# Kernel optimization log

Hardware: AMD Instinct MI355X
Metric: run time of the kernel (lower is better)

Reference implementation:

```python
import jax, jax.numpy as jnp
import numpy as np

EMBED_DIM = 256
NUM_HEADS = 8
MLP_HIDDEN = 1024
EPS = 1e-5
ROPE_BASE = 10000.0
NEG_INF = -1e9


def _ln(x, g, b):
    m = jnp.mean(x, axis=-1, keepdims=True)
    v = jnp.mean((x - m) ** 2, axis=-1, keepdims=True)
    return (x - m) / jnp.sqrt(v + EPS) * g + b


def _proj_qkv(x, W, b):
    # x: (B, L, E); W: (3E, E)
    qkv = x @ W.T + b
    q, k, v = jnp.split(qkv, 3, axis=-1)
    B, L, E = x.shape
    def h(t):
        return t.reshape(B, L, NUM_HEADS, E // NUM_HEADS).transpose(0, 2, 1, 3)
    return h(q), h(k), h(v)


def _rope(x, offset):
    # x: (B, H, L, hd), interleaved even/odd rotation
    hd = x.shape[-1]
    L = x.shape[-2]
    inv_freq = 1.0 / (ROPE_BASE ** (jnp.arange(0, hd, 2, dtype=jnp.float32) / hd))
    t = jnp.arange(L, dtype=jnp.float32) + offset
    freqs = t[:, None] * inv_freq[None, :]  # (L, hd/2)
    cos = jnp.cos(freqs)[None, None].astype(x.dtype)
    sin = jnp.sin(freqs)[None, None].astype(x.dtype)
    xe = x[..., 0::2]
    xo = x[..., 1::2]
    xr = jnp.stack((xe * cos - xo * sin, xe * sin + xo * cos), axis=-1)
    return xr.reshape(x.shape)


def _sdpa(q, k, v, bias):
    scale = 1.0 / jnp.sqrt(jnp.asarray(q.shape[-1], q.dtype))
    s = jnp.einsum('bhqd,bhkd->bhqk', q, k) * scale + bias
    p = jax.nn.softmax(s, axis=-1)
    return jnp.einsum('bhqk,bhkd->bhqd', p, v)


def _mha_self(x, in_w, in_b, out_w, out_b):
    q, k, v = _proj_qkv(x, in_w, in_b)
    o = _sdpa(q, k, v, jnp.zeros((), x.dtype))
    B, H, L, hd = o.shape
    o = o.transpose(0, 2, 1, 3).reshape(B, L, H * hd)
    return o @ out_w.T + out_b


def setup_inputs() -> dict:
    key = jax.random.key(0)
    ks = jax.random.split(key, 20)
    E, Hm = EMBED_DIM, MLP_HIDDEN
    sc = 0.02
    inp = {
        'src': jax.random.normal(ks[0], (8, 128, 64, E), dtype=jnp.float32),
        'src_mask': jax.random.randint(ks[1], (8, 128), 0, 2, dtype=jnp.int32),
        'ctx_qry_split_index': 96,
        'y_in_w': jax.random.normal(ks[2], (3 * E, E)) * sc,
        'y_in_b': jnp.zeros((3 * E,)),
        'y_out_w': jax.random.normal(ks[3], (E, E)) * sc,
        'y_out_b': jnp.zeros((E,)),
        'x_in_w': jax.random.normal(ks[4], (3 * E, E)) * sc,
        'x_in_b': jnp.zeros((3 * E,)),
        'x_out_w': jax.random.normal(ks[5], (E, E)) * sc,
        'x_out_b': jnp.zeros((E,)),
        'w1': jax.random.normal(ks[6], (Hm, E)) * sc,
        'b1': jnp.zeros((Hm,)),
        'w2': jax.random.normal(ks[7], (E, Hm)) * sc,
        'b2': jnp.zeros((E,)),
        'n1_g': jnp.ones((E,)), 'n1_b': jnp.zeros((E,)),
        'n2_g': jnp.ones((E,)), 'n2_b': jnp.zeros((E,)),
        'n3_g': jnp.ones((E,)), 'n3_b': jnp.zeros((E,)),
    }
    return inp


def reference(src, src_mask, ctx_qry_split_index,
              y_in_w, y_in_b, y_out_w, y_out_b,
              x_in_w, x_in_b, x_out_w, x_out_b,
              w1, b1, w2, b2,
              n1_g, n1_b, n2_g, n2_b, n3_g, n3_b):
    bs, R, C, E = src.shape
    S = int(ctx_qry_split_index)
    # ---- y (column-axis) self-attention ----
    x = src.reshape(bs * R, C, E)
    x = jnp.nan_to_num(x, nan=0.0, posinf=0.0, neginf=0.0)
    x = _mha_self(x, y_in_w, y_in_b, y_out_w, y_out_b) + x
    x = x.reshape(bs, R, C, E)
    x = _ln(x, n1_g, n1_b)
    # ---- x (row-axis) attention with ctx/qry split ----
    x = x.transpose(0, 2, 1, 3).reshape(bs * C, R, E)
    x = jnp.nan_to_num(x, nan=0.0, posinf=0.0, neginf=0.0)
    mask_x = jnp.broadcast_to((src_mask > 0)[:, None, :], (bs, C, R)).reshape(bs * C, R)
    kpm_ctx = ~mask_x[:, :S]  # (B, S) True = padded
    bias = jnp.where(kpm_ctx[:, None, None, :], jnp.asarray(NEG_INF, x.dtype), 0.0)
    src_ctx = x[:, :S, :]
    src_qry = x[:, S:, :]
    # ctx self-attention
    q_c, k_c, v_c = _proj_qkv(src_ctx, x_in_w, x_in_b)
    q_c = _rope(q_c, 0)
    k_c = _rope(k_c, 0)
    out_ctx = _sdpa(q_c, k_c, v_c, bias)
    B = bs * C
    out_ctx = out_ctx.transpose(0, 2, 1, 3).reshape(B, S, E)
    out_ctx = out_ctx @ x_out_w.T + x_out_b
    src_ctx = out_ctx + src_ctx
    # qry cross-attention into (updated) ctx
    q_q, _, _ = _proj_qkv(src_qry, x_in_w, x_in_b)
    _, k_c2, v_c2 = _proj_qkv(src_ctx, x_in_w, x_in_b)
    q_q = _rope(q_q, S)
    k_c2 = _rope(k_c2, 0)
    out_qry = _sdpa(q_q, k_c2, v_c2, bias)
    L_qry = R - S
    out_qry = out_qry.transpose(0, 2, 1, 3).reshape(B, L_qry, E)
    out_qry = out_qry @ x_out_w.T + x_out_b
    src_qry = out_qry + src_qry
    x = jnp.concatenate([src_ctx, src_qry], axis=1)
    x = x.reshape(bs, C, R, E).transpose(0, 2, 1, 3)
    x = _ln(x, n2_g, n2_b)
    # ---- FFN ----
    mlp = (jax.nn.gelu(x @ w1.T + b1, approximate=False)) @ w2.T + b2
    x = x + mlp
    return _ln(x, n3_g, n3_b)
```

## Files before the change

### kernel.cpp

```cpp
#include <hip/hip_runtime.h>
#include <hip/hip_bf16.h>
#include <math.h>


#define EDIM 256
#define HD   32
#define SCTX 96

typedef __bf16 bf16x8 __attribute__((ext_vector_type(8)));
typedef float  f32x4  __attribute__((ext_vector_type(4)));
union Frag { bf16x8 v; unsigned short u[8]; };

static __device__ __forceinline__ float b2f(unsigned short u) {
    return __uint_as_float(((unsigned int)u) << 16);
}
static __device__ __forceinline__ unsigned short f2b(float f) {
    unsigned int u = __float_as_uint(f);
    u += 0x7fffu + ((u >> 16) & 1u);
    return (unsigned short)(u >> 16);
}

static __device__ __forceinline__ void gload16(const unsigned short* g, unsigned short* l) {
    __builtin_amdgcn_global_load_lds(
        (const __attribute__((address_space(1))) unsigned int*)g,
        (__attribute__((address_space(3))) unsigned int*)l,
        16, 0, 0);
}

__global__ void detect_kernel(const unsigned int* __restrict__ n1g_raw,
                              int* __restrict__ flag) {
    *flag = (*n1g_raw == 0x3F800000u) ? 1 : 0;
}

struct PtrTable { const void* p[18]; };

__global__ void cvt_kernel(PtrTable t, const int* __restrict__ flag,
                           unsigned short* __restrict__ wp) {
    const int seg_off[19] = {0, 196608, 197376, 262912, 263168, 459776, 460544,
                             526080, 526336, 788480, 789504, 1051648, 1051904,
                             1052160, 1052416, 1052672, 1052928, 1053184, 1053440};
    const int f = *flag;
    int idx = blockIdx.x * blockDim.x + threadIdx.x;
    int stride = gridDim.x * blockDim.x;
    for (int i = idx; i < 1053440; i += stride) {
        int s = 0;
        while (i >= seg_off[s + 1]) ++s;
        int j = i - seg_off[s];
        unsigned short o;
        if (f) o = f2b(((const float*)t.p[s])[j]);
        else   o = ((const unsigned short*)t.p[s])[j];
        wp[i] = o;
    }
}

__global__ void rope_tab_kernel(float2* __restrict__ tab) {
    int i = blockIdx.x * blockDim.x + threadIdx.x;
    int pos = i >> 4, f = i & 15;
    float invf = exp2f((float)f * -0.8304820237193385f);
    float ang = (float)pos * invf;
    tab[i] = make_float2(__cosf(ang), __sinf(ang));
}

__global__ void prep_kernel(const void* __restrict__ src,
                            unsigned short* __restrict__ dst,
                            const int* __restrict__ flag, int n4) {
    const int f = *flag;
    int idx = blockIdx.x * blockDim.x + threadIdx.x;
    int stride = gridDim.x * blockDim.x;
    if (f) {
        const float4* s4 = (const float4*)src;
        for (int i = idx; i < n4; i += stride) {
            float4 v = s4[i];
            ushort4 o;
            o.x = ((__float_as_uint(v.x) & 0x7F800000u) == 0x7F800000u) ? 0 : f2b(v.x);
            o.y = ((__float_as_uint(v.y) & 0x7F800000u) == 0x7F800000u) ? 0 : f2b(v.y);
            o.z = ((__float_as_uint(v.z) & 0x7F800000u) == 0x7F800000u) ? 0 : f2b(v.z);
            o.w = ((__float_as_uint(v.w) & 0x7F800000u) == 0x7F800000u) ? 0 : f2b(v.w);
            ((ushort4*)dst)[i] = o;
        }
    } else {
        const ushort4* s4 = (const ushort4*)src;
        for (int i = idx; i < n4; i += stride) {
            ushort4 v = s4[i];
            if ((v.x & 0x7F80u) == 0x7F80u) v.x = 0;
            if ((v.y & 0x7F80u) == 0x7F80u) v.y = 0;
            if ((v.z & 0x7F80u) == 0x7F80u) v.z = 0;
            if ((v.w & 0x7F80u) == 0x7F80u) v.w = 0;
            ((ushort4*)dst)[i] = v;
        }
    }
}

template<int BK>
__global__ __launch_bounds__(256) void gemm_mfma(
        const unsigned short* __restrict__ A, int lda,
        const unsigned short* __restrict__ W, int ldw,
        const unsigned short* __restrict__ bias,
        const unsigned short* __restrict__ res,
        unsigned short* __restrict__ out, int ldo,
        int K, int fuse, int pred, const int* __restrict__ splitp) {
    constexpr int BUFS = 256 * BK;
    __shared__ __align__(16) unsigned short SH[512 * BK];

    const int tid = threadIdx.x;

    const int nT   = gridDim.y;
    const int nwg  = gridDim.x * nT;
    const int flat = blockIdx.y * gridDim.x + blockIdx.x;
    const int cpx  = nwg >> 3;
    const int wgid = (flat & 7) * cpx + (flat >> 3);
    const int m0 = (wgid / nT) * 128;
    const int n0 = (wgid % nT) * 128;

    const int wave = tid >> 6;
    const int lane = tid & 63;
    const int wm = (wave >> 1) << 6;
    const int wn = (wave & 1) << 6;
    const int lm = lane & 15;
    const int lq = lane >> 4;

    const int rt = tid >> 3;
    const int ct = ((tid & 7) ^ ((tid >> 3) & 7)) * 8;
    const unsigned short* Ag = A + (size_t)(m0 + rt) * lda + ct;
    const unsigned short* Wg = W + (size_t)(n0 + rt) * ldw + ct;
    const size_t astep = (size_t)32 * lda, wstep = (size_t)32 * ldw;
    const int wofs = wave * 512;

    f32x4 acc[4][4] = {};
    const int nk = K / BK;

#pragma unroll
    for (int j = 0; j < 4; ++j) {
        gload16(Ag + j * astep, SH + j * 2048 + wofs);
        gload16(Wg + j * wstep, SH + BUFS / 2 + j * 2048 + wofs);
    }
    __syncthreads();

    const int rs64 = lm & 7;
    int cur = 0;
    for (int t = 0; t < nk; ++t) {
        if (t + 1 < nk) {
            const int kn = (t + 1) * BK;
            unsigned short* Ad = SH + (cur ^ 1) * BUFS + wofs;
#pragma unroll
            for (int j = 0; j < 4; ++j) {
                gload16(Ag + j * astep + kn, Ad + j * 2048);
                gload16(Wg + j * wstep + kn, Ad + BUFS / 2 + j * 2048);
            }
        }
        const unsigned short* As = SH + cur * BUFS;
        const unsigned short* Bs = As + BUFS / 2;
#pragma unroll
        for (int kk = 0; kk < 2; ++kk) {
            bf16x8 af[4], bq[4];
#pragma unroll
            for (int i = 0; i < 4; ++i)
                af[i] = *(const bf16x8*)&As[(wm + i * 16 + lm) * 64 + (((kk * 4 + lq) ^ rs64) * 8)];
#pragma unroll
            for (int j = 0; j < 4; ++j)
                bq[j] = *(const bf16x8*)&Bs[(wn + j * 16 + lm) * 64 + (((kk * 4 + lq) ^ rs64) * 8)];
#pragma unroll
            for (int i = 0; i < 4; ++i)
#pragma unroll
                for (int j = 0; j < 4; ++j)
                    acc[i][j] = __builtin_amdgcn_mfma_f32_16x16x32_bf16(af[i], bq[j], acc[i][j], 0, 0, 0);
        }
        __syncthreads();
        cur ^= 1;
    }

    const int S = (pred != 0) ? *splitp : 0;
    float bv[4];
#pragma unroll
    for (int j = 0; j < 4; ++j)
        bv[j] = bias ? b2f(bias[n0 + wn + j * 16 + lm]) : 0.f;

    const int srow = (wave >> 1) * 16 + lq * 4;
    const int sr2 = tid >> 3;
    const int cc = (tid & 7) * 16;
    const int mH = (sr2 >> 4) * 64 + (sr2 & 15);

#pragma unroll
    for (int i = 0; i < 4; ++i) {
        unsigned short* Sl = SH + (i & 1) * 4352;
#pragma unroll
        for (int j = 0; j < 4; ++j)
#pragma unroll
            for (int r = 0; r < 4; ++r) {
                float x = acc[i][j][r] + bv[j];
                if (fuse == 1) x = 0.5f * x * (1.0f + erff(x * 0.70710678118654752f));
                Sl[(srow + r) * 136 + wn + j * 16 + lm] = f2b(x);
            }
        __syncthreads();
        {
            const int m = m0 + mH + i * 16;
            const int rr = m & 127;
            bool st = true;
            if (pred == 1 && rr >= S) st = false;
            if (pred == 2 && rr < S) st = false;
            if (st) {
#pragma unroll
                for (int h = 0; h < 2; ++h) {
                    uint4 v = *(const uint4*)&Sl[sr2 * 136 + cc + h * 8];
                    if (res) {
                        uint4 rv = *(const uint4*)(res + (size_t)m * 256 + n0 + cc + h * 8);
                        unsigned short* pv = (unsigned short*)&v;
                        const unsigned short* pr = (const unsigned short*)&rv;
#pragma unroll
                        for (int e = 0; e < 8; ++e)
                            pv[e] = f2b(b2f(pv[e]) + b2f(pr[e]));
                    }
                    *(uint4*)(out + (size_t)m * ldo + n0 + cc + h * 8) = v;
                }
            }
        }
    }
}

static __device__ __forceinline__ void rope8t(float* t, const float2* __restrict__ cs) {
#pragma unroll
    for (int p = 0; p < 4; ++p) {
        float c = cs[p].x, s = cs[p].y;
        float xe = t[2 * p], xo = t[2 * p + 1];
        t[2 * p]     = xe * c - xo * s;
        t[2 * p + 1] = xe * s + xo * c;
    }
}

template<int NQT, int NKT, bool ROPE, bool BIAS>
__global__ __launch_bounds__(64) void attn_mfma(unsigned short* __restrict__ QKV,
                                                const int* __restrict__ mask,
                                                const float2* __restrict__ tab,
                                                int seqlen, int qoff) {
    constexpr int NK = NKT * 16;
    constexpr int KS = NK / 32;
    const int s = blockIdx.x;
    const int h = blockIdx.y;
    const int lane = threadIdx.x;
    const int lm = lane & 15;
    const int lq = lane >> 4;
    const size_t rowbase = (size_t)s * seqlen;
    const float scale = 0.17677669529663689f;

    __shared__ __align__(16) unsigned short Vs[NK][40];
    __shared__ __align__(16) unsigned short Pt[16][104];
    __shared__ float bias_s[NK];

#pragma unroll
    for (int r0 = 0; r0 < NK; r0 += 16) {
        int r = r0 + (lane >> 2);
        int c = (lane & 3) * 8;
        uint4 v = *(const uint4*)(QKV + (rowbase + r) * 768 + 512 + h * 32 + c);
        *(uint4*)&Vs[r][c] = v;
    }
    if (BIAS) {
        const int b = s >> 6;
        for (int r = lane; r < NK; r += 64)
            bias_s[r] = (mask[b * 128 + r] > 0) ? 0.f : -1e9f;
    }
    Frag kf[NKT];
#pragma unroll
    for (int nt = 0; nt < NKT; ++nt) {
        const int krow = nt * 16 + lm;
        const unsigned short* kp = QKV + (rowbase + krow) * 768 + 256 + h * 32 + lq * 8;
        float t[8];
#pragma unroll
        for (int j = 0; j < 8; ++j) t[j] = b2f(kp[j]);
        if (ROPE) rope8t(t, tab + (krow << 4) + lq * 4);
#pragma unroll
        for (int j = 0; j < 8; ++j) kf[nt].u[j] = f2b(t[j]);
    }
    __syncthreads();
    Frag bvf[KS][2];
#pragma unroll
    for (int ks = 0; ks < KS; ++ks)
#pragma unroll
        for (int dt = 0; dt < 2; ++dt)
#pragma unroll
            for (int j = 0; j < 8; ++j)
                bvf[ks][dt].u[j] = Vs[ks * 32 + lq * 8 + j][dt * 16 + lm];

    for (int mt = 0; mt < NQT; ++mt) {
        Frag qf;
        const int qrow = qoff + mt * 16 + lm;
        {
            const unsigned short* qp = QKV + (rowbase + qrow) * 768 + h * 32 + lq * 8;
            float t[8];
#pragma unroll
            for (int j = 0; j < 8; ++j) t[j] = b2f(qp[j]);
            if (ROPE) rope8t(t, tab + (qrow << 4) + lq * 4);
#pragma unroll
            for (int j = 0; j < 8; ++j) qf.u[j] = f2b(t[j]);
        }
        f32x4 sacc[NKT] = {};
#pragma unroll
        for (int nt = 0; nt < NKT; ++nt)
            sacc[nt] = __builtin_amdgcn_mfma_f32_16x16x32_bf16(qf.v, kf[nt].v, sacc[nt], 0, 0, 0);
        float pv[NKT][4], mx[4], sm[4], inv[4];
#pragma unroll
        for (int r = 0; r < 4; ++r) mx[r] = -3.0e38f;
#pragma unroll
        for (int nt = 0; nt < NKT; ++nt)
#pragma unroll
            for (int r = 0; r < 4; ++r) {
                float x = sacc[nt][r] * scale;
                if (BIAS) x += bias_s[nt * 16 + lm];
                pv[nt][r] = x;
                mx[r] = fmaxf(mx[r], x);
            }
#pragma unroll
        for (int m = 1; m < 16; m <<= 1)
#pragma unroll
            for (int r = 0; r < 4; ++r) mx[r] = fmaxf(mx[r], __shfl_xor(mx[r], m, 64));
#pragma unroll
        for (int r = 0; r < 4; ++r) sm[r] = 0.f;
#pragma unroll
        for (int nt = 0; nt < NKT; ++nt)
#pragma unroll
            for (int r = 0; r < 4; ++r) {
                float p = __expf(pv[nt][r] - mx[r]);
                pv[nt][r] = p;
                sm[r] += p;
            }
#pragma unroll
        for (int m = 1; m < 16; m <<= 1)
#pragma unroll
            for (int r = 0; r < 4; ++r) sm[r] += __shfl_xor(sm[r], m, 64);
#pragma unroll
        for (int r = 0; r < 4; ++r) inv[r] = 1.f / sm[r];
#pragma unroll
        for (int nt = 0; nt < NKT; ++nt)
#pragma unroll
            for (int r = 0; r < 4; ++r)
                Pt[lq * 4 + r][nt * 16 + lm] = f2b(pv[nt][r] * inv[r]);
        __syncthreads();
        f32x4 oacc[2] = {};
#pragma unroll
        for (int ks = 0; ks < KS; ++ks) {
            Frag af;
            af.v = *(const bf16x8*)&Pt[lm][ks * 32 + lq * 8];
#pragma unroll
            for (int dt = 0; dt < 2; ++dt)
                oacc[dt] = __builtin_amdgcn_mfma_f32_16x16x32_bf16(af.v, bvf[ks][dt].v, oacc[dt], 0, 0, 0);
        }
#pragma unroll
        for (int dt = 0; dt < 2; ++dt)
#pragma unroll
            for (int r = 0; r < 4; ++r) {
                const int m = qoff + mt * 16 + lq * 4 + r;
                QKV[(rowbase + m) * 768 + h * 32 + dt * 16 + lm] = f2b(oacc[dt][r]);
            }
        __syncthreads();
    }
}

__global__ __launch_bounds__(256) void ln_permute_kernel(
        const unsigned short* __restrict__ X,
        const unsigned short* __restrict__ gam,
        const unsigned short* __restrict__ bet,
        void* __restrict__ Y, int mode, const int* __restrict__ flag) {
    const int t = (blockIdx.x << 2) + (threadIdx.x >> 6);
    const int tid = threadIdx.x & 63;
    const int e = tid << 2;
    ushort4 xv = *(const ushort4*)(X + (size_t)t * EDIM + e);
    float v0 = b2f(xv.x), v1 = b2f(xv.y), v2 = b2f(xv.z), v3 = b2f(xv.w);
    float s = v0 + v1 + v2 + v3;
#pragma unroll
    for (int m = 32; m > 0; m >>= 1) s += __shfl_xor(s, m, 64);
    float mean = s * (1.f / EDIM);
    float d0 = v0 - mean, d1 = v1 - mean, d2 = v2 - mean, d3 = v3 - mean;
    float q = d0 * d0 + d1 * d1 + d2 * d2 + d3 * d3;
#pragma unroll
    for (int m = 32; m > 0; m >>= 1) q += __shfl_xor(q, m, 64);
    float rstd = rsqrtf(q * (1.f / EDIM) + 1e-5f);
    float g0 = b2f(gam[e]), g1 = b2f(gam[e + 1]), g2 = b2f(gam[e + 2]), g3 = b2f(gam[e + 3]);
    float b0 = b2f(bet[e]), b1 = b2f(bet[e + 1]), b2_ = b2f(bet[e + 2]), b3 = b2f(bet[e + 3]);
    float y0 = d0 * rstd * g0 + b0;
    float y1 = d1 * rstd * g1 + b1;
    float y2 = d2 * rstd * g2 + b2_;
    float y3 = d3 * rstd * g3 + b3;
    size_t drow;
    if (mode == 0) {
        int b = t >> 13, r = (t >> 6) & 127, c = t & 63;
        drow = ((size_t)b << 13) + ((size_t)c << 7) + (size_t)r;
    } else if (mode == 1) {
        int b = t >> 13, c = (t >> 7) & 63, r = t & 127;
        drow = ((size_t)b << 13) + ((size_t)r << 6) + (size_t)c;
    } else {
        drow = (size_t)t;
    }
    if (mode == 2 && *flag) {
        float4 o4 = make_float4(y0, y1, y2, y3);
        *(float4*)((float*)Y + drow * EDIM + e) = o4;
    } else {
        ushort4 o;
        o.x = f2b(y0); o.y = f2b(y1); o.z = f2b(y2); o.w = f2b(y3);
        *(ushort4*)((unsigned short*)Y + drow * EDIM + e) = o;
    }
}

extern "C" void kernel_launch(void* const* d_in, const int* in_sizes, int n_in,
                              void* d_out, int out_size, void* d_ws, size_t ws_size,
                              hipStream_t stream) {
    (void)in_sizes; (void)n_in; (void)out_size; (void)ws_size;
    const void* src  = d_in[0];
    const int*  mask = (const int*)d_in[1];
    const int*  split= (const int*)d_in[2];

    int*            flag = (int*)d_ws;
    unsigned short* wp   = (unsigned short*)((char*)d_ws + 1024);
    float2*         rtab = (float2*)((char*)d_ws + (size_t)3 * 1024 * 1024);
    unsigned short* Xa   = (unsigned short*)((char*)d_ws + (size_t)4 * 1024 * 1024);
    unsigned short* Xb   = Xa + (size_t)16777216;
    unsigned short* QKV  = Xb + (size_t)16777216;
    unsigned short* HID  = QKV;

    const unsigned short* y_in_w  = wp + 0;
    const unsigned short* y_in_b  = wp + 196608;
    const unsigned short* y_out_w = wp + 197376;
    const unsigned short* y_out_b = wp + 262912;
    const unsigned short* x_in_w  = wp + 263168;
    const unsigned short* x_in_b  = wp + 459776;
    const unsigned short* x_out_w = wp + 460544;
    const unsigned short* x_out_b = wp + 526080;
    const unsigned short* w1      = wp + 526336;
    const unsigned short* b1      = wp + 788480;
    const unsigned short* w2      = wp + 789504;
    const unsigned short* b2      = wp + 1051648;
    const unsigned short* n1_g    = wp + 1051904;
    const unsigned short* n1_b    = wp + 1052160;
    const unsigned short* n2_g    = wp + 1052416;
    const unsigned short* n2_b    = wp + 1052672;
    const unsigned short* n3_g    = wp + 1052928;
    const unsigned short* n3_b    = wp + 1053184;

    detect_kernel<<<1, 1, 0, stream>>>((const unsigned int*)d_in[15], flag);

    PtrTable pt;
    for (int i = 0; i < 18; ++i) pt.p[i] = d_in[3 + i];
    cvt_kernel<<<512, 256, 0, stream>>>(pt, flag, wp);
    rope_tab_kernel<<<8, 256, 0, stream>>>(rtab);

    prep_kernel<<<4096, 256, 0, stream>>>(src, Xa, flag, 4194304);
    gemm_mfma<64><<<dim3(512, 6), 256, 0, stream>>>(Xa, 256, y_in_w, 256, y_in_b, nullptr, QKV, 768, 256, 0, 0, nullptr);
    attn_mfma<4, 4, false, false><<<dim3(1024, 8), 64, 0, stream>>>(QKV, mask, rtab, 64, 0);
    gemm_mfma<64><<<dim3(512, 2), 256, 0, stream>>>(QKV, 768, y_out_w, 256, y_out_b, Xa, Xa, 256, 256, 0, 0, nullptr);
    ln_permute_kernel<<<16384, 256, 0, stream>>>(Xa, n1_g, n1_b, Xb, 0, flag);
    gemm_mfma<64><<<dim3(512, 6), 256, 0, stream>>>(Xb, 256, x_in_w, 256, x_in_b, nullptr, QKV, 768, 256, 0, 0, nullptr);
    attn_mfma<6, 6, true, true><<<dim3(512, 8), 64, 0, stream>>>(QKV, mask, rtab, 128, 0);
    gemm_mfma<64><<<dim3(512, 2), 256, 0, stream>>>(QKV, 768, x_out_w, 256, x_out_b, Xb, Xb, 256, 256, 0, 1, split);
    gemm_mfma<64><<<dim3(512, 4), 256, 0, stream>>>(Xb, 256, x_in_w + 65536, 256, x_in_b + 256, nullptr, QKV + 256, 768, 256, 0, 0, nullptr);
    attn_mfma<2, 6, true, true><<<dim3(512, 8), 64, 0, stream>>>(QKV, mask, rtab, 128, 96);
    gemm_mfma<64><<<dim3(512, 2), 256, 0, stream>>>(QKV, 768, x_out_w, 256, x_out_b, Xb, Xb, 256, 256, 0, 2, split);
    ln_permute_kernel<<<16384, 256, 0, stream>>>(Xb, n2_g, n2_b, Xa, 1, flag);
    gemm_mfma<64><<<dim3(512, 4), 256, 0, stream>>>(Xa, 256, w1, 256, b1, nullptr, HID, 512, 256, 1, 0, nullptr);
    gemm_mfma<64><<<dim3(512, 2), 256, 0, stream>>>(HID, 512, w2, 1024, b2, Xa, Xb, 256, 512, 0, 0, nullptr);
    gemm_mfma<64><<<dim3(512, 4), 256, 0, stream>>>(Xa, 256, w1 + 512 * 256, 256, b1 + 512, nullptr, HID, 512, 256, 1, 0, nullptr);
    gemm_mfma<64><<<dim3(512, 2), 256, 0, stream>>>(HID, 512, w2 + 512, 1024, nullptr, Xb, Xb, 256, 512, 0, 0, nullptr);
    ln_permute_kernel<<<16384, 256, 0, stream>>>(Xb, n3_g, n3_b, d_out, 2, flag);
}
```

Measured before the change: 708.8 us.

## Enlarge GEMM tiles to 256x256 with 8 waves and BK=32

Restructures the MFMA GEMM from 128x128 tiles with 4 waves and BK=64 to 256x256 tiles with 8 waves (2x4 layout, 128x64 per wave) and BK=32 double buffering. The sync moves to the start of each k-step, and the epilogue is staged through LDS in 32-row chunks. The aim is more operand reuse per LDS load and fewer global reloads of A and W. In exchange each thread holds 128 accumulator floats, which raises register pressure, the grid shrinks to 256-768 workgroups, and smaller k-steps mean more barriers.

```diff
diff --git a/kernel.cpp b/kernel.cpp
--- a/kernel.cpp
+++ b/kernel.cpp
@@ -91,16 +91,14 @@
     }
 }
 
-template<int BK>
-__global__ __launch_bounds__(256) void gemm_mfma(
+__global__ __launch_bounds__(512, 2) void gemm_mfma(
         const unsigned short* __restrict__ A, int lda,
         const unsigned short* __restrict__ W, int ldw,
         const unsigned short* __restrict__ bias,
         const unsigned short* __restrict__ res,
         unsigned short* __restrict__ out, int ldo,
         int K, int fuse, int pred, const int* __restrict__ splitp) {
-    constexpr int BUFS = 256 * BK;
-    __shared__ __align__(16) unsigned short SH[512 * BK];
+    __shared__ __align__(16) unsigned short SH[32768];
 
     const int tid = threadIdx.x;
 
@@ -109,109 +107,106 @@
     const int flat = blockIdx.y * gridDim.x + blockIdx.x;
     const int cpx  = nwg >> 3;
     const int wgid = (flat & 7) * cpx + (flat >> 3);
-    const int m0 = (wgid / nT) * 128;
-    const int n0 = (wgid % nT) * 128;
+    const int m0 = (wgid / nT) * 256;
+    const int n0 = (wgid % nT) * 256;
 
     const int wave = tid >> 6;
     const int lane = tid & 63;
-    const int wm = (wave >> 1) << 6;
-    const int wn = (wave & 1) << 6;
+    const int wr = wave >> 2;
+    const int wc = wave & 3;
     const int lm = lane & 15;
     const int lq = lane >> 4;
 
-    const int rt = tid >> 3;
-    const int ct = ((tid & 7) ^ ((tid >> 3) & 7)) * 8;
+    const int rt = tid >> 2;
+    const int ct = (((tid & 3) ^ ((tid >> 3) & 3)) * 8);
     const unsigned short* Ag = A + (size_t)(m0 + rt) * lda + ct;
     const unsigned short* Wg = W + (size_t)(n0 + rt) * ldw + ct;
-    const size_t astep = (size_t)32 * lda, wstep = (size_t)32 * ldw;
+    const size_t astep = (size_t)128 * lda, wstep = (size_t)128 * ldw;
     const int wofs = wave * 512;
 
-    f32x4 acc[4][4] = {};
-    const int nk = K / BK;
-
-#pragma unroll
-    for (int j = 0; j < 4; ++j) {
-        gload16(Ag + j * astep, SH + j * 2048 + wofs);
-        gload16(Wg + j * wstep, SH + BUFS / 2 + j * 2048 + wofs);
+    f32x4 acc[8][4] = {};
+    const int nk = K >> 5;
+
+#pragma unroll
+    for (int j = 0; j < 2; ++j) {
+        gload16(Ag + j * astep, SH + j * 4096 + wofs);
+        gload16(Wg + j * wstep, SH + 8192 + j * 4096 + wofs);
+    }
+
+    const int ko = (lq ^ ((lm >> 1) & 3)) * 8;
+    for (int t = 0; t < nk; ++t) {
+        __syncthreads();
+        if (t + 1 < nk) {
+            const int kn = (t + 1) << 5;
+            unsigned short* D = SH + ((t + 1) & 1) * 16384 + wofs;
+#pragma unroll
+            for (int j = 0; j < 2; ++j) {
+                gload16(Ag + j * astep + kn, D + j * 4096);
+                gload16(Wg + j * wstep + kn, D + 8192 + j * 4096);
+            }
+        }
+        const unsigned short* As = SH + (t & 1) * 16384;
+        const unsigned short* Bs = As + 8192;
+        bf16x8 af[8], bq[4];
+#pragma unroll
+        for (int j = 0; j < 4; ++j)
+            bq[j] = *(const bf16x8*)&Bs[(wc * 64 + j * 16 + lm) * 32 + ko];
+#pragma unroll
+        for (int i = 0; i < 8; ++i)
+            af[i] = *(const bf16x8*)&As[(wr * 128 + i * 16 + lm) * 32 + ko];
+#pragma unroll
+        for (int i = 0; i < 8; ++i)
+#pragma unroll
+            for (int j = 0; j < 4; ++j)
+                acc[i][j] = __builtin_amdgcn_mfma_f32_16x16x32_bf16(af[i], bq[j], acc[i][j], 0, 0, 0);
     }
     __syncthreads();
-
-    const int rs64 = lm & 7;
-    int cur = 0;
-    for (int t = 0; t < nk; ++t) {
-        if (t + 1 < nk) {
-            const int kn = (t + 1) * BK;
-            unsigned short* Ad = SH + (cur ^ 1) * BUFS + wofs;
-#pragma unroll
-            for (int j = 0; j < 4; ++j) {
-                gload16(Ag + j * astep + kn, Ad + j * 2048);
-                gload16(Wg + j * wstep + kn, Ad + BUFS / 2 + j * 2048);
-            }
-        }
-        const unsigned short* As = SH + cur * BUFS;
-        const unsigned short* Bs = As + BUFS / 2;
-#pragma unroll
-        for (int kk = 0; kk < 2; ++kk) {
-            bf16x8 af[4], bq[4];
-#pragma unroll
-            for (int i = 0; i < 4; ++i)
-                af[i] = *(const bf16x8*)&As[(wm + i * 16 + lm) * 64 + (((kk * 4 + lq) ^ rs64) * 8)];
-#pragma unroll
-            for (int j = 0; j < 4; ++j)
-                bq[j] = *(const bf16x8*)&Bs[(wn + j * 16 + lm) * 64 + (((kk * 4 + lq) ^ rs64) * 8)];
-#pragma unroll
-            for (int i = 0; i < 4; ++i)
-#pragma unroll
-                for (int j = 0; j < 4; ++j)
-                    acc[i][j] = __builtin_amdgcn_mfma_f32_16x16x32_bf16(af[i], bq[j], acc[i][j], 0, 0, 0);
-        }
-        __syncthreads();
-        cur ^= 1;
-    }
 
     const int S = (pred != 0) ? *splitp : 0;
     float bv[4];
 #pragma unroll
     for (int j = 0; j < 4; ++j)
-        bv[j] = bias ? b2f(bias[n0 + wn + j * 16 + lm]) : 0.f;
-
-    const int srow = (wave >> 1) * 16 + lq * 4;
-    const int sr2 = tid >> 3;
-    const int cc = (tid & 7) * 16;
-    const int mH = (sr2 >> 4) * 64 + (sr2 & 15);
-
-#pragma unroll
-    for (int i = 0; i < 4; ++i) {
-        unsigned short* Sl = SH + (i & 1) * 4352;
-#pragma unroll
-        for (int j = 0; j < 4; ++j)
-#pragma unroll
-            for (int r = 0; r < 4; ++r) {
-                float x = acc[i][j][r] + bv[j];
-                if (fuse == 1) x = 0.5f * x * (1.0f + erff(x * 0.70710678118654752f));
-                Sl[(srow + r) * 136 + wn + j * 16 + lm] = f2b(x);
-            }
+        bv[j] = bias ? b2f(bias[n0 + wc * 64 + j * 16 + lm]) : 0.f;
+
+    const int rl = tid >> 5;
+    const int cc = (tid & 31) * 8;
+
+#pragma unroll
+    for (int ci = 0; ci < 8; ++ci) {
+        unsigned short* Sl = SH + (ci & 1) * 8448;
+        if (wr == (ci >> 2)) {
+            const int ib = (ci & 3) * 2;
+#pragma unroll
+            for (int il = 0; il < 2; ++il)
+#pragma unroll
+                for (int j = 0; j < 4; ++j)
+#pragma unroll
+                    for (int r = 0; r < 4; ++r) {
+                        float x = acc[ib + il][j][r] + bv[j];
+                        if (fuse == 1) x = 0.5f * x * (1.0f + erff(x * 0.70710678118654752f));
+                        Sl[(il * 16 + lq * 4 + r) * 264 + wc * 64 + j * 16 + lm] = f2b(x);
+                    }
+        }
         __syncthreads();
-        {
-            const int m = m0 + mH + i * 16;
+#pragma unroll
+        for (int h = 0; h < 2; ++h) {
+            const int row = rl + h * 16;
+            const int m = m0 + ci * 32 + row;
             const int rr = m & 127;
             bool st = true;
             if (pred == 1 && rr >= S) st = false;
             if (pred == 2 && rr < S) st = false;
             if (st) {
-#pragma unroll
-                for (int h = 0; h < 2; ++h) {
-                    uint4 v = *(const uint4*)&Sl[sr2 * 136 + cc + h * 8];
-                    if (res) {
-                        uint4 rv = *(const uint4*)(res + (size_t)m * 256 + n0 + cc + h * 8);
-                        unsigned short* pv = (unsigned short*)&v;
-                        const unsigned short* pr = (const unsigned short*)&rv;
-#pragma unroll
-                        for (int e = 0; e < 8; ++e)
-                            pv[e] = f2b(b2f(pv[e]) + b2f(pr[e]));
-                    }
-                    *(uint4*)(out + (size_t)m * ldo + n0 + cc + h * 8) = v;
+                uint4 v = *(const uint4*)&Sl[row * 264 + cc];
+                if (res) {
+                    uint4 rv = *(const uint4*)(res + (size_t)m * 256 + n0 + cc);
+                    unsigned short* pv = (unsigned short*)&v;
+                    const unsigned short* pr = (const unsigned short*)&rv;
+#pragma unroll
+                    for (int e = 0; e < 8; ++e)
+                        pv[e] = f2b(b2f(pv[e]) + b2f(pr[e]));
                 }
+                *(uint4*)(out + (size_t)m * ldo + n0 + cc) = v;
             }
         }
     }
@@ -442,20 +437,20 @@
     rope_tab_kernel<<<8, 256, 0, stream>>>(rtab);
 
     prep_kernel<<<4096, 256, 0, stream>>>(src, Xa, flag, 4194304);
-    gemm_mfma<64><<<dim3(512, 6), 256, 0, stream>>>(Xa, 256, y_in_w, 256, y_in_b, nullptr, QKV, 768, 256, 0, 0, nullptr);
+    gemm_mfma<<<dim3(256, 3), 512, 0, stream>>>(Xa, 256, y_in_w, 256, y_in_b, nullptr, QKV, 768, 256, 0, 0, nullptr);
     attn_mfma<4, 4, false, false><<<dim3(1024, 8), 64, 0, stream>>>(QKV, mask, rtab, 64, 0);
-    gemm_mfma<64><<<dim3(512, 2), 256, 0, stream>>>(QKV, 768, y_out_w, 256, y_out_b, Xa, Xa, 256, 256, 0, 0, nullptr);
+    gemm_mfma<<<dim3(256, 1), 512, 0, stream>>>(QKV, 768, y_out_w, 256, y_out_b, Xa, Xa, 256, 256, 0, 0, nullptr);
     ln_permute_kernel<<<16384, 256, 0, stream>>>(Xa, n1_g, n1_b, Xb, 0, flag);
-    gemm_mfma<64><<<dim3(512, 6), 256, 0, stream>>>(Xb, 256, x_in_w, 256, x_in_b, nullptr, QKV, 768, 256, 0, 0, nullptr);
+    gemm_mfma<<<dim3(256, 3), 512, 0, stream>>>(Xb, 256, x_in_w, 256, x_in_b, nullptr, QKV, 768, 256, 0, 0, nullptr);
     attn_mfma<6, 6, true, true><<<dim3(512, 8), 64, 0, stream>>>(QKV, mask, rtab, 128, 0);
-    gemm_mfma<64><<<dim3(512, 2), 256, 0, stream>>>(QKV, 768, x_out_w, 256, x_out_b, Xb, Xb, 256, 256, 0, 1, split);
-    gemm_mfma<64><<<dim3(512, 4), 256, 0, stream>>>(Xb, 256, x_in_w + 65536, 256, x_in_b + 256, nullptr, QKV + 256, 768, 256, 0, 0, nullptr);
+    gemm_mfma<<<dim3(256, 1), 512, 0, stream>>>(QKV, 768, x_out_w, 256, x_out_b, Xb, Xb, 256, 256, 0, 1, split);
+    gemm_mfma<<<dim3(256, 2), 512, 0, stream>>>(Xb, 256, x_in_w + 65536, 256, x_in_b + 256, nullptr, QKV + 256, 768, 256, 0, 0, nullptr);
     attn_mfma<2, 6, true, true><<<dim3(512, 8), 64, 0, stream>>>(QKV, mask, rtab, 128, 96);
-    gemm_mfma<64><<<dim3(512, 2), 256, 0, stream>>>(QKV, 768, x_out_w, 256, x_out_b, Xb, Xb, 256, 256, 0, 2, split);
+    gemm_mfma<<<dim3(256, 1), 512, 0, stream>>>(QKV, 768, x_out_w, 256, x_out_b, Xb, Xb, 256, 256, 0, 2, split);
     ln_permute_kernel<<<16384, 256, 0, stream>>>(Xb, n2_g, n2_b, Xa, 1, flag);
-    gemm_mfma<64><<<dim3(512, 4), 256, 0, stream>>>(Xa, 256, w1, 256, b1, nullptr, HID, 512, 256, 1, 0, nullptr);
-    gemm_mfma<64><<<dim3(512, 2), 256, 0, stream>>>(HID, 512, w2, 1024, b2, Xa, Xb, 256, 512, 0, 0, nullptr);
-    gemm_mfma<64><<<dim3(512, 4), 256, 0, stream>>>(Xa, 256, w1 + 512 * 256, 256, b1 + 512, nullptr, HID, 512, 256, 1, 0, nullptr);
-    gemm_mfma<64><<<dim3(512, 2), 256, 0, stream>>>(HID, 512, w2 + 512, 1024, nullptr, Xb, Xb, 256, 512, 0, 0, nullptr);
+    gemm_mfma<<<dim3(256, 2), 512, 0, stream>>>(Xa, 256, w1, 256, b1, nullptr, HID, 512, 256, 1, 0, nullptr);
+    gemm_mfma<<<dim3(256, 1), 512, 0, stream>>>(HID, 512, w2, 1024, b2, Xa, Xb, 256, 512, 0, 0, nullptr);
+    gemm_mfma<<<dim3(256, 2), 512, 0, stream>>>(Xa, 256, w1 + 512 * 256, 256, b1 + 512, nullptr, HID, 512, 256, 1, 0, nullptr);
+    gemm_mfma<<<dim3(256, 1), 512, 0, stream>>>(HID, 512, w2 + 512, 1024, nullptr, Xb, Xb, 256, 512, 0, 0, nullptr);
     ln_permute_kernel<<<16384, 256, 0, stream>>>(Xb, n3_g, n3_b, d_out, 2, flag);
 }
```

After: 1.003 ms. 1.41x slower.
